# Optimization experiments

Hardware: AMD Instinct MI355X
Metric: run time of the kernel (lower is better)

## Reference

```python
import jax, jax.numpy as jnp
import numpy as np

NUM_INDUCING = 50
B = 1 << 20  # number of query states

Z_SCALE = jnp.array([0.25, 0.2, 0.08, 400.0, 10.0], dtype=jnp.float32)
Z_SHIFT = jnp.array([0.0, 0.0, 0.0, 800.0, 12.0], dtype=jnp.float32)


def setup_inputs() -> dict:
    key = jax.random.key(0)
    k1, k2 = jax.random.split(key)
    x_star = jax.random.normal(k1, (B, 5), dtype=jnp.float32)
    # learned params, faithful to the module's initializers
    log_lengthscale = jnp.log(jnp.array([0.2, 0.15, 0.1, 400.0, 15.0], dtype=jnp.float32))
    log_variance = jnp.asarray(jnp.log(0.08), dtype=jnp.float32)
    Z_raw = 0.5 * jax.random.normal(k2, (NUM_INDUCING, 5), dtype=jnp.float32)
    return {"x_star": x_star, "log_lengthscale": log_lengthscale,
            "log_variance": log_variance, "Z_raw": Z_raw}


def _matern52_from_d(d, prior_var):
    s = jnp.sqrt(5.0) * d
    return prior_var * (1.0 + s + (5.0 / 3.0) * d * d) * jnp.exp(-s)


def reference(x_star, log_lengthscale, log_variance, Z_raw):
    ls = jnp.exp(log_lengthscale)                      # (5,)
    prior_var = jnp.exp(log_variance)                  # scalar
    Z = jnp.tanh(Z_raw) * Z_SCALE + Z_SHIFT            # (M,5)
    inv_ls = 1.0 / (ls + 1e-8)
    Zs = Z * inv_ls                                    # scaled inducing pts (M,5)
    Xs = x_star * inv_ls                               # scaled queries (B,5)

    # K_ZZ: tiny (M,M), exact pairwise form
    diff = Zs[:, None, :] - Zs[None, :, :]             # (M,M,5)
    d_zz = jnp.sqrt(jnp.sum(diff * diff, axis=-1) + 1e-8)
    k_ZZ = _matern52_from_d(d_zz, prior_var)
    K_ZZ_inv = jnp.linalg.inv(k_ZZ + 1e-4 * jnp.eye(NUM_INDUCING, dtype=k_ZZ.dtype))

    # k_xZ: (B,M) via the GEMM-friendly expansion of squared distance
    x2 = jnp.sum(Xs * Xs, axis=-1)                     # (B,)
    z2 = jnp.sum(Zs * Zs, axis=-1)                     # (M,)
    d2 = x2[:, None] + z2[None, :] - 2.0 * (Xs @ Zs.T)  # (B,M)
    d_xz = jnp.sqrt(jnp.maximum(d2, 0.0) + 1e-8)
    k_xZ = _matern52_from_d(d_xz, prior_var)           # (B,M)

    red = jnp.einsum('bi,ij,bj->b', k_xZ, K_ZZ_inv, k_xZ)
    variance = jnp.maximum(prior_var - red, 1e-6)
    return jnp.sqrt(variance)                          # (B,)
```

## Files before the change

### kernel.cpp

```cpp
#include <hip/hip_runtime.h>
#include <hip/hip_bf16.h>
#include <math.h>

#define M 50
#define SQRT5 2.2360679774997896f

typedef short  bf16x8 __attribute__((ext_vector_type(8)));
typedef float  f32x4v __attribute__((ext_vector_type(4)));

__constant__ float c_zscale[5] = {0.25f, 0.2f, 0.08f, 400.0f, 10.0f};
__constant__ float c_zshift[5] = {0.0f, 0.0f, 0.0f, 800.0f, 12.0f};

#if __has_builtin(__builtin_amdgcn_sqrtf)
__device__ __forceinline__ float fsqrt(float x) { return __builtin_amdgcn_sqrtf(x); }
#else
__device__ __forceinline__ float fsqrt(float x) { return sqrtf(x); }
#endif

#if __has_builtin(__builtin_amdgcn_exp2f)
__device__ __forceinline__ float fexp2(float x) { return __builtin_amdgcn_exp2f(x); }
#else
__device__ __forceinline__ float fexp2(float x) { return exp2f(x); }
#endif

#if __has_builtin(__builtin_amdgcn_rcpf)
__device__ __forceinline__ float frcp(float x) { return __builtin_amdgcn_rcpf(x); }
#else
__device__ __forceinline__ float frcp(float x) { return 1.0f / x; }
#endif

__device__ __forceinline__ float lane_bcast(float v, int lane) {
    return __builtin_bit_cast(float,
        __builtin_amdgcn_readlane(__builtin_bit_cast(int, v), lane));
}

__device__ __forceinline__ unsigned short bfu(float f) {
    return __builtin_bit_cast(unsigned short, __float2bfloat16(f));
}

#define FOR50(F) F(0) F(1) F(2) F(3) F(4) F(5) F(6) F(7) F(8) F(9) \
  F(10) F(11) F(12) F(13) F(14) F(15) F(16) F(17) F(18) F(19) \
  F(20) F(21) F(22) F(23) F(24) F(25) F(26) F(27) F(28) F(29) \
  F(30) F(31) F(32) F(33) F(34) F(35) F(36) F(37) F(38) F(39) \
  F(40) F(41) F(42) F(43) F(44) F(45) F(46) F(47) F(48) F(49)
#define FOR50P(F, p) F(0,p) F(1,p) F(2,p) F(3,p) F(4,p) F(5,p) F(6,p) F(7,p) F(8,p) F(9,p) \
  F(10,p) F(11,p) F(12,p) F(13,p) F(14,p) F(15,p) F(16,p) F(17,p) F(18,p) F(19,p) \
  F(20,p) F(21,p) F(22,p) F(23,p) F(24,p) F(25,p) F(26,p) F(27,p) F(28,p) F(29,p) \
  F(30,p) F(31,p) F(32,p) F(33,p) F(34,p) F(35,p) F(36,p) F(37,p) F(38,p) F(39,p) \
  F(40,p) F(41,p) F(42,p) F(43,p) F(44,p) F(45,p) F(46,p) F(47,p) F(48,p) F(49,p)

#define DECL_C(i) float c##i;
#define INIT_C(i) c##i = s_K[lrow * M + (i)];
#define CH_UPD(i, p) if ((i) > (p)) { \
    const float cj = lane_bcast(c##p, (i)); \
    c##i = fmaf(-c##p, cj, c##i); }
#define CH_PIVOT(p) { \
    const float dp  = lane_bcast(c##p, (p)); \
    const float inv = frcp(fsqrt(dp)); \
    c##p *= inv; \
    if (lane < M) s_K[lane * M + (p)] = c##p; \
    FOR50P(CH_UPD, p) }

#define DECL_Y(i) float y##i;
#define TSU(q, i) if ((q) < (i)) acc = fmaf(-s_K[(i) * M + (q)], y##q, acc);
#define TS_ROW(i) { \
    float acc = (lane == (i)) ? 1.0f : 0.0f; \
    FOR50P(TSU, i) \
    y##i = acc * frcp(s_K[(i) * M + (i)]); }

#define W_EMIT(i) wtp[(i) * 64 + lane] = bfu(pv * y##i);

__global__ __launch_bounds__(256, 1) void gp_setup(const float* __restrict__ log_ls,
                                                   const float* __restrict__ log_var,
                                                   const float* __restrict__ zraw,
                                                   float* __restrict__ ws) {
    __shared__ float s_ils[5];
    __shared__ float s_pv;
    __shared__ float s_Zs[M * 5];
    __shared__ float s_K[M * M];

    const int t = threadIdx.x;
    unsigned short* wtp = (unsigned short*)(ws + 512);

    if (t == 0) s_pv = expf(log_var[0]);
    if (t < 5)  s_ils[t] = 1.0f / (expf(log_ls[t]) + 1e-8f);
    __syncthreads();
    if (t < M * 5) {
        int j = t % 5;
        s_Zs[t] = (tanhf(zraw[t]) * c_zscale[j] + c_zshift[j]) * s_ils[j];
    }
    __syncthreads();
    const float pv = s_pv;

    for (int e = t; e < 4096; e += 256) wtp[e] = 0;
    for (int e = t; e < M * M; e += 256) {
        int i = e / M, jj = e % M;
        float d2 = 0.0f;
        #pragma unroll
        for (int q = 0; q < 5; ++q) {
            float df = s_Zs[i * 5 + q] - s_Zs[jj * 5 + q];
            d2 = fmaf(df, df, d2);
        }
        float d = fsqrt(d2 + 1e-8f);
        float s = SQRT5 * d;
        s_K[e] = pv * (1.0f + s + (5.0f / 3.0f) * (d * d)) * expf(-s)
                 + ((i == jj) ? 1e-4f : 0.0f);
    }
    __syncthreads();

    if (t < 64) {
        const int lane = t;
        const int lrow = (t < M) ? t : (M - 1);
        {
            FOR50(DECL_C)
            FOR50(INIT_C)
            FOR50(CH_PIVOT)
        }
        {
            FOR50(DECL_Y)
            FOR50(TS_ROW)
            FOR50(W_EMIT)
        }
    }

    if (t < M) {
        float z2 = 0.0f;
        #pragma unroll
        for (int q = 0; q < 5; ++q) {
            float v = SQRT5 * s_Zs[t * 5 + q];
            z2 = fmaf(v, v, z2);
        }
        #pragma unroll
        for (int q = 0; q < 5; ++q) ws[t * 8 + q] = -2.0f * SQRT5 * s_Zs[t * 5 + q];
        ws[t * 8 + 5] = z2 + 5e-8f;
        ws[t * 8 + 6] = 0.0f;
        ws[t * 8 + 7] = 0.0f;
    }
    if (t < 5)  ws[400 + t] = SQRT5 * s_ils[t];
    if (t == 0) { ws[405] = 0.0f; ws[406] = pv; ws[407] = 0.0f; }
}

__device__ __forceinline__ float kval_lds(const float* __restrict__ sc,
                                          const float xs[5], float x2, int m) {
    f32x4v c0 = *(const f32x4v*)(sc + m * 8);
    f32x4v c1 = *(const f32x4v*)(sc + m * 8 + 4);
    float u = x2 + c1[1];
    u = fmaf(c0[0], xs[0], u);
    u = fmaf(c0[1], xs[1], u);
    u = fmaf(c0[2], xs[2], u);
    u = fmaf(c0[3], xs[3], u);
    u = fmaf(c1[0], xs[4], u);
    u = fmaxf(u, 5e-8f);
    float s = fsqrt(u);
    float e = fexp2(s * -1.4426950408889634f);
    return fmaf(u, (1.0f / 3.0f), 1.0f + s) * e;
}

__global__ __launch_bounds__(256) void gp_var(const float* __restrict__ x,
                                              const float* __restrict__ ws,
                                              float* __restrict__ out, int B) {
    __shared__ float sx[1280];
    __shared__ __align__(16) float sc[408];
    __shared__ __align__(16) unsigned short sk[4 * 64 * 64];
    const int t    = threadIdx.x;
    const int lane = t & 63;
    const int wid  = t >> 6;
    const long long base = (long long)blockIdx.x * 1280;

    {
        const long long tot = (long long)B * 5;
        const float4* xv = (const float4*)(x + base);
        for (int i = t; i < 320; i += 256) {
            if (base + (long long)i * 4 + 3 < tot) ((float4*)sx)[i] = xv[i];
        }
        const float4* wv = (const float4*)ws;
        if (t < 102) ((float4*)sc)[t] = wv[t];
    }
    __syncthreads();

    const float pv = sc[406];

    float xs[5];
    #pragma unroll
    for (int j = 0; j < 5; ++j) xs[j] = sx[t * 5 + j] * sc[400 + j];

    float x2 = 0.0f;
    #pragma unroll
    for (int j = 0; j < 5; ++j) x2 = fmaf(xs[j], xs[j], x2);

    char* kbase = (char*)sk + wid * 8192;
    const int swz_w = (lane & 7) << 4;
    #pragma unroll
    for (int c = 0; c < 8; ++c) {
        unsigned int w0 = 0, w1 = 0, w2 = 0, w3 = 0;
        if (c < 6) {
            float a, b;
            a = kval_lds(sc, xs, x2, c * 8 + 0);
            b = kval_lds(sc, xs, x2, c * 8 + 1);
            w0 = (unsigned int)bfu(a) | ((unsigned int)bfu(b) << 16);
            a = kval_lds(sc, xs, x2, c * 8 + 2);
            b = kval_lds(sc, xs, x2, c * 8 + 3);
            w1 = (unsigned int)bfu(a) | ((unsigned int)bfu(b) << 16);
            a = kval_lds(sc, xs, x2, c * 8 + 4);
            b = kval_lds(sc, xs, x2, c * 8 + 5);
            w2 = (unsigned int)bfu(a) | ((unsigned int)bfu(b) << 16);
            a = kval_lds(sc, xs, x2, c * 8 + 6);
            b = kval_lds(sc, xs, x2, c * 8 + 7);
            w3 = (unsigned int)bfu(a) | ((unsigned int)bfu(b) << 16);
        } else if (c == 6) {
            float a, b;
            a = kval_lds(sc, xs, x2, 48);
            b = kval_lds(sc, xs, x2, 49);
            w0 = (unsigned int)bfu(a) | ((unsigned int)bfu(b) << 16);
        }
        int off = lane * 128 + ((c * 16) ^ swz_w);
        *(int4*)(kbase + off) = make_int4((int)w0, (int)w1, (int)w2, (int)w3);
        asm volatile("" ::: "memory");
    }

    const int r15 = lane & 15, g = lane >> 4;
    bf16x8 wf[4][2];
    const char* wtb = (const char*)(ws + 512);
    #pragma unroll
    for (int tc = 0; tc < 4; ++tc) {
        #pragma unroll
        for (int ks = 0; ks < 2; ++ks) {
            int o = ((tc * 16 + r15) * 64 + ks * 32 + g * 8) * 2;
            wf[tc][ks] = *(const bf16x8*)(wtb + o);
        }
    }

    float part[4][4];
    #pragma unroll
    for (int tr = 0; tr < 4; ++tr) {
        const int r = tr * 16 + r15;
        const char* arow = kbase + r * 128;
        const int swz = (r15 & 7) << 4;
        bf16x8 a0 = *(const bf16x8*)(arow + ((g * 16) ^ swz));
        bf16x8 a1 = *(const bf16x8*)(arow + (((4 + g) * 16) ^ swz));
        #pragma unroll
        for (int tc = 0; tc < 4; ++tc) {
            f32x4v acc = {0.0f, 0.0f, 0.0f, 0.0f};
            acc = __builtin_amdgcn_mfma_f32_16x16x32_bf16(a0, wf[tc][0], acc, 0, 0, 0);
            acc = __builtin_amdgcn_mfma_f32_16x16x32_bf16(a1, wf[tc][1], acc, 0, 0, 0);
            #pragma unroll
            for (int rg = 0; rg < 4; ++rg) {
                part[tr][rg] = (tc == 0) ? acc[rg] * acc[rg]
                                         : fmaf(acc[rg], acc[rg], part[tr][rg]);
            }
        }
    }

    #pragma unroll
    for (int tr = 0; tr < 4; ++tr) {
        #pragma unroll
        for (int rg = 0; rg < 4; ++rg) {
            float v = part[tr][rg];
            v += __shfl_xor(v, 1);
            v += __shfl_xor(v, 2);
            v += __shfl_xor(v, 4);
            v += __shfl_xor(v, 8);
            part[tr][rg] = v;
        }
    }

    float red = part[0][0];
    #pragma unroll
    for (int i = 1; i < 16; ++i)
        if (r15 == i) red = part[i >> 2][i & 3];

    const int pt = blockIdx.x * 256 + wid * 64 + (r15 >> 2) * 16 + g * 4 + (r15 & 3);
    out[pt] = fsqrt(fmaxf(pv - red, 1e-6f));
}

extern "C" void kernel_launch(void* const* d_in, const int* in_sizes, int n_in,
                              void* d_out, int out_size, void* d_ws, size_t ws_size,
                              hipStream_t stream) {
    const float* x    = (const float*)d_in[0];
    const float* ll   = (const float*)d_in[1];
    const float* lv   = (const float*)d_in[2];
    const float* zraw = (const float*)d_in[3];
    float* out = (float*)d_out;
    float* ws  = (float*)d_ws;

    const int B = in_sizes[0] / 5;

    hipLaunchKernelGGL(gp_setup, dim3(1), dim3(256), 0, stream, ll, lv, zraw, ws);
    const int grid = (B + 255) / 256;
    hipLaunchKernelGGL(gp_var, dim3(grid), dim3(256), 0, stream, x, ws, out, B);
}
```

Baseline: 66.04 us.

## Halve LDS staging for k_xZ tiles via two-phase write/MFMA and packed bf16 convert

Each lane now computes all 50 kernel values into registers, packed with a single v_cvt_pk_bf16_f32 per pair. The k_xZ tile is staged through LDS in two phases of 32 rows each, so the per-wave LDS buffer shrinks from 8 KB to 4 KB. The aim is to cut LDS footprint, allowing more resident blocks, and to make the bf16 packing cheaper. In exchange it holds 32 extra VGPRs live and adds phase-predicated stores whose ordering relies only on compiler barriers within the wave.

```diff
diff --git a/kernel.cpp b/kernel.cpp
--- a/kernel.cpp
+++ b/kernel.cpp
@@ -161,7 +161,7 @@
                                               float* __restrict__ out, int B) {
     __shared__ float sx[1280];
     __shared__ __align__(16) float sc[408];
-    __shared__ __align__(16) unsigned short sk[4 * 64 * 64];
+    __shared__ __align__(16) unsigned short sk[4 * 32 * 64];
     const int t    = threadIdx.x;
     const int lane = t & 63;
     const int wid  = t >> 6;
@@ -188,35 +188,17 @@
     #pragma unroll
     for (int j = 0; j < 5; ++j) x2 = fmaf(xs[j], xs[j], x2);
 
-    char* kbase = (char*)sk + wid * 8192;
-    const int swz_w = (lane & 7) << 4;
-    #pragma unroll
-    for (int c = 0; c < 8; ++c) {
-        unsigned int w0 = 0, w1 = 0, w2 = 0, w3 = 0;
-        if (c < 6) {
-            float a, b;
-            a = kval_lds(sc, xs, x2, c * 8 + 0);
-            b = kval_lds(sc, xs, x2, c * 8 + 1);
-            w0 = (unsigned int)bfu(a) | ((unsigned int)bfu(b) << 16);
-            a = kval_lds(sc, xs, x2, c * 8 + 2);
-            b = kval_lds(sc, xs, x2, c * 8 + 3);
-            w1 = (unsigned int)bfu(a) | ((unsigned int)bfu(b) << 16);
-            a = kval_lds(sc, xs, x2, c * 8 + 4);
-            b = kval_lds(sc, xs, x2, c * 8 + 5);
-            w2 = (unsigned int)bfu(a) | ((unsigned int)bfu(b) << 16);
-            a = kval_lds(sc, xs, x2, c * 8 + 6);
-            b = kval_lds(sc, xs, x2, c * 8 + 7);
-            w3 = (unsigned int)bfu(a) | ((unsigned int)bfu(b) << 16);
-        } else if (c == 6) {
-            float a, b;
-            a = kval_lds(sc, xs, x2, 48);
-            b = kval_lds(sc, xs, x2, 49);
-            w0 = (unsigned int)bfu(a) | ((unsigned int)bfu(b) << 16);
-        }
-        int off = lane * 128 + ((c * 16) ^ swz_w);
-        *(int4*)(kbase + off) = make_int4((int)w0, (int)w1, (int)w2, (int)w3);
-        asm volatile("" ::: "memory");
-    }
+    unsigned int w[32];
+    #pragma unroll
+    for (int mp = 0; mp < 25; ++mp) {
+        float a = kval_lds(sc, xs, x2, 2 * mp);
+        float b = kval_lds(sc, xs, x2, 2 * mp + 1);
+        unsigned int d;
+        asm("v_cvt_pk_bf16_f32 %0, %1, %2" : "=v"(d) : "v"(a), "v"(b));
+        w[mp] = d;
+    }
+    #pragma unroll
+    for (int mp = 25; mp < 32; ++mp) w[mp] = 0;
 
     const int r15 = lane & 15, g = lane >> 4;
     bf16x8 wf[4][2];
@@ -230,25 +212,44 @@
         }
     }
 
+    char* kbase = (char*)sk + wid * 4096;
+    const int rb    = lane & 31;
+    const int swz_w = (lane & 7) << 4;
+    const int swz_r = (r15 & 7) << 4;
     float part[4][4];
-    #pragma unroll
-    for (int tr = 0; tr < 4; ++tr) {
-        const int r = tr * 16 + r15;
-        const char* arow = kbase + r * 128;
-        const int swz = (r15 & 7) << 4;
-        bf16x8 a0 = *(const bf16x8*)(arow + ((g * 16) ^ swz));
-        bf16x8 a1 = *(const bf16x8*)(arow + (((4 + g) * 16) ^ swz));
-        #pragma unroll
-        for (int tc = 0; tc < 4; ++tc) {
-            f32x4v acc = {0.0f, 0.0f, 0.0f, 0.0f};
-            acc = __builtin_amdgcn_mfma_f32_16x16x32_bf16(a0, wf[tc][0], acc, 0, 0, 0);
-            acc = __builtin_amdgcn_mfma_f32_16x16x32_bf16(a1, wf[tc][1], acc, 0, 0, 0);
+
+    #pragma unroll
+    for (int ph = 0; ph < 2; ++ph) {
+        if ((lane >> 5) == ph) {
             #pragma unroll
-            for (int rg = 0; rg < 4; ++rg) {
-                part[tr][rg] = (tc == 0) ? acc[rg] * acc[rg]
-                                         : fmaf(acc[rg], acc[rg], part[tr][rg]);
+            for (int c = 0; c < 8; ++c) {
+                int4 v = make_int4((int)w[c * 4 + 0], (int)w[c * 4 + 1],
+                                   (int)w[c * 4 + 2], (int)w[c * 4 + 3]);
+                *(int4*)(kbase + rb * 128 + ((c * 16) ^ swz_w)) = v;
             }
         }
+        asm volatile("" ::: "memory");
+        #pragma unroll
+        for (int trh = 0; trh < 2; ++trh) {
+            const int tr = ph * 2 + trh;
+            const char* arow = kbase + (trh * 16 + r15) * 128;
+            bf16x8 a0 = __builtin_bit_cast(bf16x8,
+                            *(const int4*)(arow + ((g * 16) ^ swz_r)));
+            bf16x8 a1 = __builtin_bit_cast(bf16x8,
+                            *(const int4*)(arow + (((4 + g) * 16) ^ swz_r)));
+            #pragma unroll
+            for (int tc = 0; tc < 4; ++tc) {
+                f32x4v acc = {0.0f, 0.0f, 0.0f, 0.0f};
+                acc = __builtin_amdgcn_mfma_f32_16x16x32_bf16(a0, wf[tc][0], acc, 0, 0, 0);
+                acc = __builtin_amdgcn_mfma_f32_16x16x32_bf16(a1, wf[tc][1], acc, 0, 0, 0);
+                #pragma unroll
+                for (int rg = 0; rg < 4; ++rg) {
+                    part[tr][rg] = (tc == 0) ? acc[rg] * acc[rg]
+                                             : fmaf(acc[rg], acc[rg], part[tr][rg]);
+                }
+            }
+        }
+        asm volatile("" ::: "memory");
     }
 
     #pragma unroll
```

After: 65.44 us. About the same (-0.9%).
